# Kernel optimization log

Measured on AMD Instinct MI355X. Metric: run time of the kernel, lower is better.

The kernel has to match this reference:

```python
import jax, jax.numpy as jnp
import numpy as np

HEADS = 8
EPS = 1e-5


def _layernorm(x, g, b):
    mu = jnp.mean(x, axis=-1, keepdims=True)
    var = jnp.mean(jnp.square(x - mu), axis=-1, keepdims=True)
    return (x - mu) * jax.lax.rsqrt(var + EPS) * g + b


def setup_inputs() -> dict:
    key = jax.random.key(0)
    ks = jax.random.split(key, 10)
    B, S, D = 4, 2048, 256
    d_ff = 2 * D
    s = 0.02
    return {
        "x": jax.random.normal(ks[0], (B, S, D), dtype=jnp.float32),
        "ln1_g": jnp.ones((D,), jnp.float32),
        "ln1_b": jnp.zeros((D,), jnp.float32),
        "w_qkv": jax.random.normal(ks[1], (3 * D, D), jnp.float32) * s,
        "b_qkv": jnp.zeros((3 * D,), jnp.float32),
        "w_proj": jax.random.normal(ks[2], (D, D), jnp.float32) * s,
        "b_proj": jnp.zeros((D,), jnp.float32),
        "ln2_g": jnp.ones((D,), jnp.float32),
        "ln2_b": jnp.zeros((D,), jnp.float32),
        "w1": jax.random.normal(ks[3], (d_ff, D), jnp.float32) * s,
        "b1": jnp.zeros((d_ff,), jnp.float32),
        "w2": jax.random.normal(ks[4], (D, d_ff), jnp.float32) * s,
        "b2": jnp.zeros((D,), jnp.float32),
    }


def reference(x, ln1_g, ln1_b, w_qkv, b_qkv, w_proj, b_proj,
              ln2_g, ln2_b, w1, b1, w2, b2):
    B, S, D = x.shape
    H = HEADS
    dh = D // H
    scale = dh ** -0.5

    # --- attention sublayer (pre-LN) ---
    y = _layernorm(x, ln1_g, ln1_b)
    qkv = y @ w_qkv.T + b_qkv                       # [B,S,3D]
    qkv = qkv.reshape(B, S, 3, H, dh)
    q = jnp.transpose(qkv[:, :, 0], (0, 2, 1, 3))   # [B,H,S,dh]
    k = jnp.transpose(qkv[:, :, 1], (0, 2, 1, 3))
    v = jnp.transpose(qkv[:, :, 2], (0, 2, 1, 3))
    attn = jax.nn.softmax(jnp.einsum('bhsd,bhtd->bhst', q, k) * scale, axis=-1)
    ctx = jnp.einsum('bhst,bhtd->bhsd', attn, v)    # [B,H,S,dh]
    ctx = jnp.transpose(ctx, (0, 2, 1, 3)).reshape(B, S, D)
    x = x + ctx @ w_proj.T + b_proj

    # --- FFN sublayer (pre-LN) ---
    y = _layernorm(x, ln2_g, ln2_b)
    h = jax.nn.silu(y @ w1.T + b1)                  # [B,S,2D]
    x = x + h @ w2.T + b2
    return x
```

## Files before the change

### kernel.cpp

```cpp
#include <hip/hip_runtime.h>
#include <cstddef>

constexpr int kB   = 4;
constexpr int kS   = 2048;
constexpr int kD   = 256;
constexpr int kH   = 8;
constexpr int kDH  = 32;
constexpr int kDFF = 512;
constexpr int kM   = kB * kS;
constexpr float kEps = 1e-5f;
constexpr float kScaleL2E = 0.17677669529663687f * 1.4426950408889634f;

typedef float f32x4  __attribute__((ext_vector_type(4)));
typedef short bf16x8 __attribute__((ext_vector_type(8)));
typedef unsigned short u16;
typedef unsigned int   u32;

__device__ inline u16 f2bf(float x) {
    union { float f; unsigned u; } c; c.f = x;
    const unsigned r = c.u + 0x7fffu + ((c.u >> 16) & 1u);
    return (u16)(r >> 16);
}

__device__ inline u32 pk_trunc(float lo, float hi) {
    union { float f; u32 u; } a, b; a.f = lo; b.f = hi;
    return __builtin_amdgcn_perm(b.u, a.u, 0x07060302u);
}

__global__ __launch_bounds__(256)
void ln_kernel(const float* __restrict__ x, const float* __restrict__ g,
               const float* __restrict__ b, u16* __restrict__ y)
{
    const int wave = threadIdx.x >> 6;
    const int lane = threadIdx.x & 63;
    const int row  = blockIdx.x * 4 + wave;
    const float4 v = *(const float4*)&x[(size_t)row * kD + lane * 4];
    float s1 = (v.x + v.y) + (v.z + v.w);
    float s2 = (v.x * v.x + v.y * v.y) + (v.z * v.z + v.w * v.w);
    #pragma unroll
    for (int off = 1; off < 64; off <<= 1) {
        s1 += __shfl_xor(s1, off);
        s2 += __shfl_xor(s2, off);
    }
    const float mu  = s1 * (1.0f / kD);
    const float var = s2 * (1.0f / kD) - mu * mu;
    const float inv = rsqrtf(var + kEps);
    const float4 g4 = *(const float4*)&g[lane * 4];
    const float4 b4 = *(const float4*)&b[lane * 4];
    *(ushort4*)&y[(size_t)row * kD + lane * 4] = make_ushort4(
        f2bf((v.x - mu) * inv * g4.x + b4.x),
        f2bf((v.y - mu) * inv * g4.y + b4.y),
        f2bf((v.z - mu) * inv * g4.z + b4.z),
        f2bf((v.w - mu) * inv * g4.w + b4.w));
}

template<int NT, int OUTMODE, bool RES, int KTOT>
__global__ __launch_bounds__(256)
void gemm_bf16(const u16* __restrict__ A, const float* __restrict__ Wf,
               const float* __restrict__ bias, const float* __restrict__ res,
               float* __restrict__ Cf, u16* __restrict__ Cb,
               u16* __restrict__ KbP, u16* __restrict__ VtP, int N)
{
    constexpr int BSTR = KTOT + 4;
    __shared__ u16 Bs[NT * BSTR];
    const int tid  = threadIdx.x;
    const int wave = tid >> 6;
    const int lane = tid & 63;
    const int quad = lane >> 4;
    const int l16  = lane & 15;
    const int m0 = blockIdx.x * 128;
    const int n0 = blockIdx.y * NT;

    {
        constexpr int ITS = (NT * KTOT) / 1024;
        #pragma unroll
        for (int it = 0; it < ITS; ++it) {
            const int e   = it * 1024 + tid * 4;
            const int row = e / KTOT;
            const int col = e & (KTOT - 1);
            const float4 wv = *(const float4*)&Wf[(size_t)(n0 + row) * KTOT + col];
            *(ushort4*)&Bs[row * BSTR + col] = make_ushort4(
                f2bf(wv.x), f2bf(wv.y), f2bf(wv.z), f2bf(wv.w));
        }
    }
    __syncthreads();

    f32x4 acc[2][NT / 16];
    #pragma unroll
    for (int mt = 0; mt < 2; ++mt)
        #pragma unroll
        for (int ni = 0; ni < NT / 16; ++ni) acc[mt][ni] = {0.f, 0.f, 0.f, 0.f};

    const u16* arow0 = &A[(size_t)(m0 + wave * 16 + l16) * KTOT];
    const u16* arow1 = &A[(size_t)(m0 + 64 + wave * 16 + l16) * KTOT];
    #pragma unroll 4
    for (int k0 = 0; k0 < KTOT; k0 += 32) {
        const bf16x8 a0 = *(const bf16x8*)&arow0[k0 + quad * 8];
        const bf16x8 a1 = *(const bf16x8*)&arow1[k0 + quad * 8];
        #pragma unroll
        for (int ni = 0; ni < NT / 16; ++ni) {
            const bf16x8 bf = *(const bf16x8*)&Bs[(ni * 16 + l16) * BSTR + k0 + quad * 8];
            acc[0][ni] = __builtin_amdgcn_mfma_f32_16x16x32_bf16(a0, bf, acc[0][ni], 0, 0, 0);
            acc[1][ni] = __builtin_amdgcn_mfma_f32_16x16x32_bf16(a1, bf, acc[1][ni], 0, 0, 0);
        }
    }

    #pragma unroll
    for (int mt = 0; mt < 2; ++mt) {
        #pragma unroll
        for (int ni = 0; ni < NT / 16; ++ni) {
            const float bias_v = bias[n0 + ni * 16 + l16];
            #pragma unroll
            for (int r = 0; r < 4; ++r) {
                const int m = m0 + mt * 64 + wave * 16 + quad * 4 + r;
                float v = acc[mt][ni][r] + bias_v;
                if (OUTMODE == 0) {
                    const int n = n0 + ni * 16 + l16;
                    if (RES) v += res[(size_t)m * N + n];
                    Cf[(size_t)m * N + n] = v;
                } else if (OUTMODE == 1) {
                    const int n = n0 + ni * 16 + l16;
                    v = v / (1.0f + __expf(-v));
                    Cb[(size_t)m * N + n] = f2bf(v);
                } else {
                    const int rgn = n0 >> 8;
                    const int nl  = (n0 & 255) + ni * 16 + l16;
                    const int hh  = nl >> 5, dh = nl & 31;
                    const int bb  = m >> 11, s = m & (kS - 1);
                    const int bh  = bb * kH + hh;
                    if (rgn == 0)
                        Cb[((size_t)bh * kS + s) * kDH + dh] = f2bf(v * kScaleL2E);
                    else if (rgn == 1)
                        KbP[((size_t)bh * kS + s) * kDH + dh] = f2bf(v);
                    else {
                        const int so = s & 31;
                        const int vq = (so >> 2) & 3;
                        const int vj = (so & 3) | (((so >> 4) & 1) << 2);
                        VtP[(((size_t)bh * (kS / 32) + (s >> 5)) * 4 + vq) * 256
                            + dh * 8 + vj] = f2bf(v);
                    }
                }
            }
        }
    }
}

__global__ __launch_bounds__(256)
void attn_kernel(const u16* __restrict__ Qb, const u16* __restrict__ Kb,
                 const u16* __restrict__ Vp, u16* __restrict__ ctx)
{
    __shared__ float cbuf[2][64 * 33];
    const int tid  = threadIdx.x;
    const int wave = tid >> 6;
    const int lane = tid & 63;
    const int quad = lane >> 4;
    const int l16  = lane & 15;
    const int h = blockIdx.y;
    const int b = blockIdx.z;
    const int bh = b * kH + h;
    const int qsub = wave >> 1;
    const int half = wave & 1;
    const int q0 = blockIdx.x * 128 + qsub * 64;

    bf16x8 aq[4];
    #pragma unroll
    for (int qb = 0; qb < 4; ++qb)
        aq[qb] = *(const bf16x8*)
            &Qb[((size_t)bh * kS + q0 + qb * 16 + l16) * kDH + quad * 8];

    const u16* Kbase = Kb + (size_t)bh * kS * kDH;
    const u16* Vbase = Vp + (size_t)bh * (kS * 32);

    f32x4 O[4][2] = {};
    f32x4 lsum[4] = {};
    const f32x4 zz = {0.f, 0.f, 0.f, 0.f};
    union { u32 u[4]; bf16x8 v; } ones;
    ones.u[0] = ones.u[1] = ones.u[2] = ones.u[3] = 0x3F803F80u;

    auto load_tile = [&](int kt, bf16x8 (&kf)[4], bf16x8 (&vf)[2][2]) {
        #pragma unroll
        for (int kg = 0; kg < 4; ++kg)
            kf[kg] = *(const bf16x8*)
                &Kbase[(size_t)(kt + kg * 16 + l16) * kDH + quad * 8];
        #pragma unroll
        for (int ks = 0; ks < 2; ++ks)
            #pragma unroll
            for (int nf = 0; nf < 2; ++nf)
                vf[ks][nf] = *(const bf16x8*)
                    &Vbase[(size_t)(((kt >> 5) + ks) * 4 + quad) * 1024
                           + (nf * 16 + l16) * 8];
    };

    auto comp_tile = [&](bf16x8 (&kf)[4], bf16x8 (&vf)[2][2]) {
        #pragma unroll
        for (int qb = 0; qb < 4; ++qb) {
            f32x4 S0 = __builtin_amdgcn_mfma_f32_16x16x32_bf16(kf[0], aq[qb], zz, 0, 0, 0);
            f32x4 S1 = __builtin_amdgcn_mfma_f32_16x16x32_bf16(kf[1], aq[qb], zz, 0, 0, 0);
            f32x4 S2 = __builtin_amdgcn_mfma_f32_16x16x32_bf16(kf[2], aq[qb], zz, 0, 0, 0);
            f32x4 S3 = __builtin_amdgcn_mfma_f32_16x16x32_bf16(kf[3], aq[qb], zz, 0, 0, 0);

            union { u32 u[4]; bf16x8 v; } pA0, pA1;
            pA0.u[0] = pk_trunc(__builtin_amdgcn_exp2f(S0[0]), __builtin_amdgcn_exp2f(S0[1]));
            pA0.u[1] = pk_trunc(__builtin_amdgcn_exp2f(S0[2]), __builtin_amdgcn_exp2f(S0[3]));
            pA0.u[2] = pk_trunc(__builtin_amdgcn_exp2f(S1[0]), __builtin_amdgcn_exp2f(S1[1]));
            pA0.u[3] = pk_trunc(__builtin_amdgcn_exp2f(S1[2]), __builtin_amdgcn_exp2f(S1[3]));
            pA1.u[0] = pk_trunc(__builtin_amdgcn_exp2f(S2[0]), __builtin_amdgcn_exp2f(S2[1]));
            pA1.u[1] = pk_trunc(__builtin_amdgcn_exp2f(S2[2]), __builtin_amdgcn_exp2f(S2[3]));
            pA1.u[2] = pk_trunc(__builtin_amdgcn_exp2f(S3[0]), __builtin_amdgcn_exp2f(S3[1]));
            pA1.u[3] = pk_trunc(__builtin_amdgcn_exp2f(S3[2]), __builtin_amdgcn_exp2f(S3[3]));

            lsum[qb] = __builtin_amdgcn_mfma_f32_16x16x32_bf16(pA0.v, ones.v, lsum[qb], 0, 0, 0);
            lsum[qb] = __builtin_amdgcn_mfma_f32_16x16x32_bf16(pA1.v, ones.v, lsum[qb], 0, 0, 0);

            O[qb][0] = __builtin_amdgcn_mfma_f32_16x16x32_bf16(pA0.v, vf[0][0], O[qb][0], 0, 0, 0);
            O[qb][1] = __builtin_amdgcn_mfma_f32_16x16x32_bf16(pA0.v, vf[0][1], O[qb][1], 0, 0, 0);
            O[qb][0] = __builtin_amdgcn_mfma_f32_16x16x32_bf16(pA1.v, vf[1][0], O[qb][0], 0, 0, 0);
            O[qb][1] = __builtin_amdgcn_mfma_f32_16x16x32_bf16(pA1.v, vf[1][1], O[qb][1], 0, 0, 0);
        }
    };

    const int kbeg = half * (kS / 2);
    #pragma unroll 1
    for (int t2 = 0; t2 < 8; ++t2) {
        const int ktA = kbeg + t2 * 128;
        bf16x8 kfA[4], vfA[2][2], kfB[4], vfB[2][2];
        load_tile(ktA,      kfA, vfA);
        load_tile(ktA + 64, kfB, vfB);
        comp_tile(kfA, vfA);
        comp_tile(kfB, vfB);
    }

    float* cb = cbuf[qsub];
    if (half == 1) {
        #pragma unroll
        for (int qb = 0; qb < 4; ++qb)
            #pragma unroll
            for (int r = 0; r < 4; ++r) {
                const int row = qb * 16 + quad * 4 + r;
                cb[row * 33 + l16]      = O[qb][0][r];
                cb[row * 33 + 16 + l16] = O[qb][1][r];
                if (l16 == 0)
                    cb[row * 33 + 32] = lsum[qb][r];
            }
    }
    __syncthreads();
    if (half == 0) {
        #pragma unroll
        for (int qb = 0; qb < 4; ++qb)
            #pragma unroll
            for (int r = 0; r < 4; ++r) {
                const int row = qb * 16 + quad * 4 + r;
                const float lq  = lsum[qb][r] + cb[row * 33 + 32];
                const float inv = 1.0f / lq;
                const float o0 = O[qb][0][r] + cb[row * 33 + l16];
                const float o1 = O[qb][1][r] + cb[row * 33 + 16 + l16];
                const int q = q0 + row;
                u16* crow = ctx + ((size_t)(b * kS + q)) * kD + h * kDH;
                crow[l16]      = f2bf(o0 * inv);
                crow[16 + l16] = f2bf(o1 * inv);
            }
    }
}

extern "C" void kernel_launch(void* const* d_in, const int* in_sizes, int n_in,
                              void* d_out, int out_size, void* d_ws, size_t ws_size,
                              hipStream_t stream)
{
    const float* x      = (const float*)d_in[0];
    const float* ln1_g  = (const float*)d_in[1];
    const float* ln1_b  = (const float*)d_in[2];
    const float* w_qkv  = (const float*)d_in[3];
    const float* b_qkv  = (const float*)d_in[4];
    const float* w_proj = (const float*)d_in[5];
    const float* b_proj = (const float*)d_in[6];
    const float* ln2_g  = (const float*)d_in[7];
    const float* ln2_b  = (const float*)d_in[8];
    const float* w1     = (const float*)d_in[9];
    const float* b1     = (const float*)d_in[10];
    const float* w2     = (const float*)d_in[11];
    const float* b2     = (const float*)d_in[12];
    float* out = (float*)d_out;

    char* ws = (char*)d_ws;
    u16* Qb  = (u16*)ws;
    u16* Kb  = (u16*)(ws + ((size_t)4  << 20));
    u16* Vp  = (u16*)(ws + ((size_t)8  << 20));
    u16* ctx = (u16*)(ws + ((size_t)12 << 20));
    u16* y   = (u16*)(ws + ((size_t)16 << 20));
    u16* h   = (u16*)ws;

    const dim3 blk(256);

    ln_kernel<<<dim3(kM / 4), blk, 0, stream>>>(x, ln1_g, ln1_b, y);
    gemm_bf16<64, 2, false, 256><<<dim3(kM / 128, 12), blk, 0, stream>>>(
        y, w_qkv, b_qkv, nullptr, nullptr, Qb, Kb, Vp, 0);
    attn_kernel<<<dim3(kS / 128, kH, kB), blk, 0, stream>>>(Qb, Kb, Vp, ctx);
    gemm_bf16<32, 0, true, 256><<<dim3(kM / 128, kD / 32), blk, 0, stream>>>(
        ctx, w_proj, b_proj, x, out, nullptr, nullptr, nullptr, kD);
    ln_kernel<<<dim3(kM / 4), blk, 0, stream>>>(out, ln2_g, ln2_b, y);
    gemm_bf16<64, 1, false, 256><<<dim3(kM / 128, kDFF / 64), blk, 0, stream>>>(
        y, w1, b1, nullptr, nullptr, h, nullptr, nullptr, kDFF);
    gemm_bf16<32, 0, true, 512><<<dim3(kM / 128, kD / 32), blk, 0, stream>>>(
        h, w2, b2, out, out, nullptr, nullptr, nullptr, kD);
}
```

Baseline: 160.5 us.

## Fuse LayerNorm into following GEMMs by folding gamma/beta into weights and bias

Removes the two standalone LayerNorm kernels. Each LN-consuming GEMM now reads fp32 rows directly, computes row mean and variance per wave, and normalizes on the fly while packing to bf16. Gamma is folded into the weight tile and beta is folded into the bias through a W·beta dot product. This saves two launches and the bf16 intermediate write and read, but each column block now re-reads and re-reduces the fp32 A rows (12 and 8 times), and truncation replaces rounding for the activations.

```diff
diff --git a/kernel.cpp b/kernel.cpp
--- a/kernel.cpp
+++ b/kernel.cpp
@@ -27,37 +27,12 @@
     return __builtin_amdgcn_perm(b.u, a.u, 0x07060302u);
 }
 
+template<int NT, int OUTMODE, bool RES, int KTOT, bool LNA>
 __global__ __launch_bounds__(256)
-void ln_kernel(const float* __restrict__ x, const float* __restrict__ g,
-               const float* __restrict__ b, u16* __restrict__ y)
-{
-    const int wave = threadIdx.x >> 6;
-    const int lane = threadIdx.x & 63;
-    const int row  = blockIdx.x * 4 + wave;
-    const float4 v = *(const float4*)&x[(size_t)row * kD + lane * 4];
-    float s1 = (v.x + v.y) + (v.z + v.w);
-    float s2 = (v.x * v.x + v.y * v.y) + (v.z * v.z + v.w * v.w);
-    #pragma unroll
-    for (int off = 1; off < 64; off <<= 1) {
-        s1 += __shfl_xor(s1, off);
-        s2 += __shfl_xor(s2, off);
-    }
-    const float mu  = s1 * (1.0f / kD);
-    const float var = s2 * (1.0f / kD) - mu * mu;
-    const float inv = rsqrtf(var + kEps);
-    const float4 g4 = *(const float4*)&g[lane * 4];
-    const float4 b4 = *(const float4*)&b[lane * 4];
-    *(ushort4*)&y[(size_t)row * kD + lane * 4] = make_ushort4(
-        f2bf((v.x - mu) * inv * g4.x + b4.x),
-        f2bf((v.y - mu) * inv * g4.y + b4.y),
-        f2bf((v.z - mu) * inv * g4.z + b4.z),
-        f2bf((v.w - mu) * inv * g4.w + b4.w));
-}
-
-template<int NT, int OUTMODE, bool RES, int KTOT>
-__global__ __launch_bounds__(256)
-void gemm_bf16(const u16* __restrict__ A, const float* __restrict__ Wf,
-               const float* __restrict__ bias, const float* __restrict__ res,
+void gemm_bf16(const u16* __restrict__ A, const float* __restrict__ Af,
+               const float* __restrict__ lng, const float* __restrict__ lnb,
+               const float* __restrict__ Wf, const float* __restrict__ bias,
+               const float* __restrict__ res,
                float* __restrict__ Cf, u16* __restrict__ Cb,
                u16* __restrict__ KbP, u16* __restrict__ VtP, int N)
 {
@@ -78,10 +53,49 @@
             const int e   = it * 1024 + tid * 4;
             const int row = e / KTOT;
             const int col = e & (KTOT - 1);
-            const float4 wv = *(const float4*)&Wf[(size_t)(n0 + row) * KTOT + col];
+            float4 wv = *(const float4*)&Wf[(size_t)(n0 + row) * KTOT + col];
+            if constexpr (LNA) {
+                const float4 g4 = *(const float4*)&lng[col];
+                wv.x *= g4.x; wv.y *= g4.y; wv.z *= g4.z; wv.w *= g4.w;
+            }
             *(ushort4*)&Bs[row * BSTR + col] = make_ushort4(
                 f2bf(wv.x), f2bf(wv.y), f2bf(wv.z), f2bf(wv.w));
         }
+    }
+
+    const float* xr0 = nullptr; const float* xr1 = nullptr;
+    const u16*  arow0 = nullptr; const u16*  arow1 = nullptr;
+    float iv0 = 0.f, nc0 = 0.f, iv1 = 0.f, nc1 = 0.f;
+    if constexpr (LNA) {
+        xr0 = &Af[(size_t)(m0 + wave * 16 + l16) * KTOT];
+        xr1 = &Af[(size_t)(m0 + 64 + wave * 16 + l16) * KTOT];
+        float s10 = 0.f, s20 = 0.f, s11 = 0.f, s21 = 0.f;
+        #pragma unroll
+        for (int k0 = 0; k0 < KTOT; k0 += 32) {
+            const float4 a = *(const float4*)&xr0[k0 + quad * 8];
+            const float4 b = *(const float4*)&xr0[k0 + quad * 8 + 4];
+            const float4 c = *(const float4*)&xr1[k0 + quad * 8];
+            const float4 d = *(const float4*)&xr1[k0 + quad * 8 + 4];
+            s10 += (a.x + a.y) + (a.z + a.w) + (b.x + b.y) + (b.z + b.w);
+            s20 += a.x*a.x + a.y*a.y + a.z*a.z + a.w*a.w
+                 + b.x*b.x + b.y*b.y + b.z*b.z + b.w*b.w;
+            s11 += (c.x + c.y) + (c.z + c.w) + (d.x + d.y) + (d.z + d.w);
+            s21 += c.x*c.x + c.y*c.y + c.z*c.z + c.w*c.w
+                 + d.x*d.x + d.y*d.y + d.z*d.z + d.w*d.w;
+        }
+        s10 += __shfl_xor(s10, 16); s10 += __shfl_xor(s10, 32);
+        s20 += __shfl_xor(s20, 16); s20 += __shfl_xor(s20, 32);
+        s11 += __shfl_xor(s11, 16); s11 += __shfl_xor(s11, 32);
+        s21 += __shfl_xor(s21, 16); s21 += __shfl_xor(s21, 32);
+        const float mu0 = s10 * (1.0f / KTOT);
+        const float mu1 = s11 * (1.0f / KTOT);
+        iv0 = rsqrtf(s20 * (1.0f / KTOT) - mu0 * mu0 + kEps);
+        iv1 = rsqrtf(s21 * (1.0f / KTOT) - mu1 * mu1 + kEps);
+        nc0 = -mu0 * iv0;
+        nc1 = -mu1 * iv1;
+    } else {
+        arow0 = &A[(size_t)(m0 + wave * 16 + l16) * KTOT];
+        arow1 = &A[(size_t)(m0 + 64 + wave * 16 + l16) * KTOT];
     }
     __syncthreads();
 
@@ -91,17 +105,64 @@
         #pragma unroll
         for (int ni = 0; ni < NT / 16; ++ni) acc[mt][ni] = {0.f, 0.f, 0.f, 0.f};
 
-    const u16* arow0 = &A[(size_t)(m0 + wave * 16 + l16) * KTOT];
-    const u16* arow1 = &A[(size_t)(m0 + 64 + wave * 16 + l16) * KTOT];
-    #pragma unroll 4
-    for (int k0 = 0; k0 < KTOT; k0 += 32) {
-        const bf16x8 a0 = *(const bf16x8*)&arow0[k0 + quad * 8];
-        const bf16x8 a1 = *(const bf16x8*)&arow1[k0 + quad * 8];
-        #pragma unroll
-        for (int ni = 0; ni < NT / 16; ++ni) {
-            const bf16x8 bf = *(const bf16x8*)&Bs[(ni * 16 + l16) * BSTR + k0 + quad * 8];
-            acc[0][ni] = __builtin_amdgcn_mfma_f32_16x16x32_bf16(a0, bf, acc[0][ni], 0, 0, 0);
-            acc[1][ni] = __builtin_amdgcn_mfma_f32_16x16x32_bf16(a1, bf, acc[1][ni], 0, 0, 0);
+    if constexpr (LNA) {
+        #pragma unroll 2
+        for (int k0 = 0; k0 < KTOT; k0 += 32) {
+            const float4 xa = *(const float4*)&xr0[k0 + quad * 8];
+            const float4 xb = *(const float4*)&xr0[k0 + quad * 8 + 4];
+            const float4 xc = *(const float4*)&xr1[k0 + quad * 8];
+            const float4 xd = *(const float4*)&xr1[k0 + quad * 8 + 4];
+            union { u32 u[4]; bf16x8 v; } ua, ub;
+            ua.u[0] = pk_trunc(xa.x * iv0 + nc0, xa.y * iv0 + nc0);
+            ua.u[1] = pk_trunc(xa.z * iv0 + nc0, xa.w * iv0 + nc0);
+            ua.u[2] = pk_trunc(xb.x * iv0 + nc0, xb.y * iv0 + nc0);
+            ua.u[3] = pk_trunc(xb.z * iv0 + nc0, xb.w * iv0 + nc0);
+            ub.u[0] = pk_trunc(xc.x * iv1 + nc1, xc.y * iv1 + nc1);
+            ub.u[1] = pk_trunc(xc.z * iv1 + nc1, xc.w * iv1 + nc1);
+            ub.u[2] = pk_trunc(xd.x * iv1 + nc1, xd.y * iv1 + nc1);
+            ub.u[3] = pk_trunc(xd.z * iv1 + nc1, xd.w * iv1 + nc1);
+            const bf16x8 a0 = ua.v;
+            const bf16x8 a1 = ub.v;
+            #pragma unroll
+            for (int ni = 0; ni < NT / 16; ++ni) {
+                const bf16x8 bf = *(const bf16x8*)&Bs[(ni * 16 + l16) * BSTR + k0 + quad * 8];
+                acc[0][ni] = __builtin_amdgcn_mfma_f32_16x16x32_bf16(a0, bf, acc[0][ni], 0, 0, 0);
+                acc[1][ni] = __builtin_amdgcn_mfma_f32_16x16x32_bf16(a1, bf, acc[1][ni], 0, 0, 0);
+            }
+        }
+    } else {
+        #pragma unroll 4
+        for (int k0 = 0; k0 < KTOT; k0 += 32) {
+            const bf16x8 a0 = *(const bf16x8*)&arow0[k0 + quad * 8];
+            const bf16x8 a1 = *(const bf16x8*)&arow1[k0 + quad * 8];
+            #pragma unroll
+            for (int ni = 0; ni < NT / 16; ++ni) {
+                const bf16x8 bf = *(const bf16x8*)&Bs[(ni * 16 + l16) * BSTR + k0 + quad * 8];
+                acc[0][ni] = __builtin_amdgcn_mfma_f32_16x16x32_bf16(a0, bf, acc[0][ni], 0, 0, 0);
+                acc[1][ni] = __builtin_amdgcn_mfma_f32_16x16x32_bf16(a1, bf, acc[1][ni], 0, 0, 0);
+            }
+        }
+    }
+
+    float biasv[NT / 16];
+    #pragma unroll
+    for (int ni = 0; ni < NT / 16; ++ni) {
+        biasv[ni] = bias[n0 + ni * 16 + l16];
+        if constexpr (LNA) {
+            const float* wrow = &Wf[(size_t)(n0 + ni * 16 + l16) * KTOT
+                                    + quad * (KTOT / 4)];
+            const float* brow = &lnb[quad * (KTOT / 4)];
+            float accb = 0.f;
+            #pragma unroll 4
+            for (int kk = 0; kk < KTOT / 4; kk += 4) {
+                const float4 wv = *(const float4*)&wrow[kk];
+                const float4 bv = *(const float4*)&brow[kk];
+                accb += wv.x * bv.x + wv.y * bv.y;
+                accb += wv.z * bv.z + wv.w * bv.w;
+            }
+            accb += __shfl_xor(accb, 16);
+            accb += __shfl_xor(accb, 32);
+            biasv[ni] += accb;
         }
     }
 
@@ -109,7 +170,7 @@
     for (int mt = 0; mt < 2; ++mt) {
         #pragma unroll
         for (int ni = 0; ni < NT / 16; ++ni) {
-            const float bias_v = bias[n0 + ni * 16 + l16];
+            const float bias_v = biasv[ni];
             #pragma unroll
             for (int r = 0; r < 4; ++r) {
                 const int m = m0 + mt * 64 + wave * 16 + quad * 4 + r;
@@ -286,20 +347,21 @@
     u16* Kb  = (u16*)(ws + ((size_t)4  << 20));
     u16* Vp  = (u16*)(ws + ((size_t)8  << 20));
     u16* ctx = (u16*)(ws + ((size_t)12 << 20));
-    u16* y   = (u16*)(ws + ((size_t)16 << 20));
     u16* h   = (u16*)ws;
 
     const dim3 blk(256);
 
-    ln_kernel<<<dim3(kM / 4), blk, 0, stream>>>(x, ln1_g, ln1_b, y);
-    gemm_bf16<64, 2, false, 256><<<dim3(kM / 128, 12), blk, 0, stream>>>(
-        y, w_qkv, b_qkv, nullptr, nullptr, Qb, Kb, Vp, 0);
+    gemm_bf16<64, 2, false, 256, true><<<dim3(kM / 128, 12), blk, 0, stream>>>(
+        nullptr, x, ln1_g, ln1_b, w_qkv, b_qkv, nullptr,
+        nullptr, Qb, Kb, Vp, 0);
     attn_kernel<<<dim3(kS / 128, kH, kB), blk, 0, stream>>>(Qb, Kb, Vp, ctx);
-    gemm_bf16<32, 0, true, 256><<<dim3(kM / 128, kD / 32), blk, 0, stream>>>(
-        ctx, w_proj, b_proj, x, out, nullptr, nullptr, nullptr, kD);
-    ln_kernel<<<dim3(kM / 4), blk, 0, stream>>>(out, ln2_g, ln2_b, y);
-    gemm_bf16<64, 1, false, 256><<<dim3(kM / 128, kDFF / 64), blk, 0, stream>>>(
-        y, w1, b1, nullptr, nullptr, h, nullptr, nullptr, kDFF);
-    gemm_bf16<32, 0, true, 512><<<dim3(kM / 128, kD / 32), blk, 0, stream>>>(
-        h, w2, b2, out, out, nullptr, nullptr, nullptr, kD);
-}
+    gemm_bf16<32, 0, true, 256, false><<<dim3(kM / 128, kD / 32), blk, 0, stream>>>(
+        ctx, nullptr, nullptr, nullptr, w_proj, b_proj, x,
+        out, nullptr, nullptr, nullptr, kD);
+    gemm_bf16<64, 1, false, 256, true><<<dim3(kM / 128, kDFF / 64), blk, 0, stream>>>(
+        nullptr, out, ln2_g, ln2_b, w1, b1, nullptr,
+        nullptr, h, nullptr, nullptr, kDFF);
+    gemm_bf16<32, 0, true, 512, false><<<dim3(kM / 128, kD / 32), blk, 0, stream>>>(
+        h, nullptr, nullptr, nullptr, w2, b2, out,
+        out, nullptr, nullptr, nullptr, kD);
+}
```

New measurement: 225.4 us. +40.4%, slower.
